# Performance work log

Measured on AMD Instinct MI355X. Metric: run time of the kernel, lower is better.

## Reference

```python
import jax, jax.numpy as jnp
import numpy as np

B, N, D, H, E = 16, 512, 256, 8, 16
DH = D // H
NEG = -1e9


def setup_inputs() -> dict:
    key = jax.random.key(0)
    ks = jax.random.split(key, 12)
    s = 0.02
    return {
        "h": jax.random.normal(ks[0], (B, N, D), dtype=jnp.float32),
        "edges": jax.random.normal(ks[1], (B, N, N, E), dtype=jnp.float32),
        "dense_mask": jnp.ones((B, N, N), dtype=bool),
        "mask": jnp.ones((B, N), dtype=bool),
        "Wq": jax.random.normal(ks[2], (D, D), dtype=jnp.float32) * s,
        "bq": jnp.zeros((D,), dtype=jnp.float32),
        "Wk": jax.random.normal(ks[3], (D, D), dtype=jnp.float32) * s,
        "bk": jnp.zeros((D,), dtype=jnp.float32),
        "Wv": jax.random.normal(ks[4], (D, D), dtype=jnp.float32) * s,
        "bv": jnp.zeros((D,), dtype=jnp.float32),
        "Wo": jax.random.normal(ks[5], (D, D), dtype=jnp.float32) * s,
        "bo": jnp.zeros((D,), dtype=jnp.float32),
        "Wp": jax.random.normal(ks[6], (E, H), dtype=jnp.float32) * s,
        "bp": jnp.zeros((H,), dtype=jnp.float32),
    }


def reference(h, edges, dense_mask, mask, Wq, bq, Wk, bk, Wv, bv, Wo, bo, Wp, bp):
    # content Q/K/V projections, split into heads
    q = (h @ Wq + bq).reshape(B, N, H, DH)
    k = (h @ Wk + bk).reshape(B, N, H, DH)
    v = (h @ Wv + bv).reshape(B, N, H, DH)
    # scaled content scores [B,H,N,N]
    scores = jnp.einsum("bnhd,bmhd->bhnm", q, k) / jnp.sqrt(jnp.float32(DH))
    # PositionAttention: per-head edge bias from the dense edge stack
    pos = jnp.einsum("bnme,eh->bhnm", edges, Wp) + bp[None, :, None, None]
    pos = pos / jnp.sqrt(jnp.float32(H))  # scale_attention
    scores = scores + pos  # merge_attention: sum (bias injected into scores)
    # fuse edge mask (dense_mask) with key padding mask (~mask is attn_mask)
    valid = dense_mask[:, None, :, :] & mask[:, None, None, :]
    scores = jnp.where(valid, scores, NEG)
    attn = jax.nn.softmax(scores, axis=-1)
    out = jnp.einsum("bhnm,bmhd->bnhd", attn, v).reshape(B, N, D)
    out = out @ Wo + bo
    return out, attn
```

## Files before the change

### kernel.cpp

```cpp
#include <hip/hip_runtime.h>
#include <hip/hip_bf16.h>

constexpr int kB = 16, kN = 512, kD = 256, kH = 8, kE = 16, kDH = 32;

typedef float f4 __attribute__((ext_vector_type(4)));
typedef __bf16 bf8 __attribute__((ext_vector_type(8)));

__device__ __forceinline__ void gload16(const void* g, const void* l) {
  __builtin_amdgcn_global_load_lds(
      (const __attribute__((address_space(1))) void*)g,
      (__attribute__((address_space(3))) void*)l, 16, 0, 0);
}

__global__ __launch_bounds__(256) void cast_h_kernel(const float* __restrict__ h,
                                                     __bf16* __restrict__ hb) {
  const int idx = (blockIdx.x * 256 + threadIdx.x) * 8;
  f4 a = *(const f4*)(h + idx);
  f4 b = *(const f4*)(h + idx + 4);
  bf8 o;
  o[0] = (__bf16)a[0]; o[1] = (__bf16)a[1]; o[2] = (__bf16)a[2]; o[3] = (__bf16)a[3];
  o[4] = (__bf16)b[0]; o[5] = (__bf16)b[1]; o[6] = (__bf16)b[2]; o[7] = (__bf16)b[3];
  *(bf8*)(hb + idx) = o;
}

__global__ __launch_bounds__(256) void prep_w_kernel(
    const float* __restrict__ Wq, const float* __restrict__ Wk,
    const float* __restrict__ Wv, const float* __restrict__ Wo,
    __bf16* __restrict__ Wt, __bf16* __restrict__ Wot) {
  const int r = blockIdx.x;
  const int t = threadIdx.x;
  if (r < 768) {
    const float* src = (r < 256) ? Wq : (r < 512) ? Wv : Wv;
    src = (r < 256) ? Wq : (r < 512) ? Wk : Wv;
    const int c = r & 255;
    Wt[(size_t)r * 256 + t] = (__bf16)src[(size_t)t * 256 + c];
  } else {
    const int rr = r - 768;
    Wot[(size_t)rr * 256 + t] = (__bf16)Wo[(size_t)t * 256 + rr];
  }
}

__global__ __launch_bounds__(256) void prep_pos_kernel(
    const float* __restrict__ edges, const int* __restrict__ dmask,
    const int* __restrict__ kmask, const float* __restrict__ Wp,
    const float* __restrict__ bp, unsigned int* __restrict__ posp) {
  const int bn = blockIdx.x;
  const int b = bn >> 9;
  const int n = bn & 511;
  const int tid = threadIdx.x;

  __shared__ __align__(16) float stg[8192];
  __shared__ __align__(16) unsigned int prow[2048];

  const float* rowg = edges + (size_t)bn * (kN * kE);

#pragma unroll
  for (int j = 0; j < 8; ++j) {
    const int L = j * 4096 + tid * 16;
    const int c = L >> 6;
    const int s = (L >> 4) & 3;
    const int e4 = s ^ (c & 3);
    gload16(rowg + c * 16 + e4 * 4, (const char*)stg + L);
  }
  __asm__ __volatile__("s_waitcnt vmcnt(0)" ::: "memory");
  __builtin_amdgcn_s_barrier();

  const float RS8 = 0.35355339059327373f;
  float bph[8];
#pragma unroll
  for (int hh = 0; hh < 8; ++hh) bph[hh] = bp[hh] * RS8;

#pragma unroll
  for (int half = 0; half < 2; ++half) {
    const int c = half * 256 + tid;
    const int dm = dmask[(size_t)bn * kN + c];
    const int km = kmask[b * kN + c];
    const bool valid = (dm != 0) && (km != 0);

    float acc[8];
#pragma unroll
    for (int hh = 0; hh < 8; ++hh) acc[hh] = 0.f;
#pragma unroll
    for (int e4 = 0; e4 < 4; ++e4) {
      const int s = e4 ^ (c & 3);
      f4 ev = *(const f4*)(stg + c * 16 + s * 4);
#pragma unroll
      for (int i = 0; i < 4; ++i) {
        const float e_ = ev[i];
#pragma unroll
        for (int hh = 0; hh < 8; ++hh)
          acc[hh] = fmaf(e_, Wp[(e4 * 4 + i) * kH + hh], acc[hh]);
      }
    }

    unsigned int w[4];
#pragma unroll
    for (int pp = 0; pp < 4; ++pp) {
      const float lo = valid ? fmaf(acc[2 * pp], RS8, bph[2 * pp]) : -1e9f;
      const float hi = valid ? fmaf(acc[2 * pp + 1], RS8, bph[2 * pp + 1]) : -1e9f;
      union { __bf16 h2[2]; unsigned int u; } pk;
      pk.h2[0] = (__bf16)lo;
      pk.h2[1] = (__bf16)hi;
      w[pp] = pk.u;
    }
    const int rot = (c + (c >> 3)) & 3;
    uint4 v;
    ((unsigned int*)&v)[0] = w[(0 - rot) & 3];
    ((unsigned int*)&v)[1] = w[(1 - rot) & 3];
    ((unsigned int*)&v)[2] = w[(2 - rot) & 3];
    ((unsigned int*)&v)[3] = w[(3 - rot) & 3];
    *(uint4*)&prow[c * 4] = v;
  }
  __builtin_amdgcn_s_barrier();

#pragma unroll
  for (int it = 0; it < 8; ++it) {
    const int li = it * 256 + tid;
    const int pp = li >> 9;
    const int m = li & 511;
    const int rot = (m + (m >> 3)) & 3;
    const unsigned int val = prow[m * 4 + ((pp + rot) & 3)];
    posp[((((size_t)(b * 4 + pp) * kN) + n) << 9) + m] = val;
  }
}

__global__ __launch_bounds__(256, 4) void qkv_gemm_kernel(
    const __bf16* __restrict__ hb, const __bf16* __restrict__ Wt,
    const float* __restrict__ bq, const float* __restrict__ bk,
    const float* __restrict__ bv,
    __bf16* __restrict__ qw, __bf16* __restrict__ kw, __bf16* __restrict__ vtw) {
  const int M0 = blockIdx.x * 128;
  const int N0 = blockIdx.y * 64;
  const int tid = threadIdx.x;
  const int wave = tid >> 6, lane = tid & 63;
  const int l15 = lane & 15, lq = lane >> 4;
  const int wm = wave & 1, wn = wave >> 1;
  const f4 fzero = {0.f, 0.f, 0.f, 0.f};

  f4 acc[4][2];
#pragma unroll
  for (int tm = 0; tm < 4; ++tm)
#pragma unroll
    for (int tn = 0; tn < 2; ++tn) acc[tm][tn] = fzero;

#pragma unroll
  for (int kk = 0; kk < 256; kk += 32) {
    bf8 af[4], bfr[2];
#pragma unroll
    for (int tm = 0; tm < 4; ++tm)
      af[tm] = *(const bf8*)(hb + (size_t)(M0 + wm * 64 + tm * 16 + l15) * 256 + kk + lq * 8);
#pragma unroll
    for (int tn = 0; tn < 2; ++tn)
      bfr[tn] = *(const bf8*)(Wt + (size_t)(N0 + wn * 32 + tn * 16 + l15) * 256 + kk + lq * 8);
#pragma unroll
    for (int tm = 0; tm < 4; ++tm)
#pragma unroll
      for (int tn = 0; tn < 2; ++tn)
        acc[tm][tn] = __builtin_amdgcn_mfma_f32_16x16x32_bf16(af[tm], bfr[tn], acc[tm][tn], 0, 0, 0);
  }

  const float QS = 0.17677669529663687f;
  const int wsel = N0 >> 8;
#pragma unroll
  for (int tn = 0; tn < 2; ++tn) {
    const int n = N0 + wn * 32 + tn * 16 + l15;
    const int c = n & 255;
    const float bias = (wsel == 0) ? bq[c] : (wsel == 1) ? bk[c] : bv[c];
#pragma unroll
    for (int tm = 0; tm < 4; ++tm) {
#pragma unroll
      for (int r = 0; r < 4; ++r) {
        const int m = M0 + wm * 64 + tm * 16 + lq * 4 + r;
        const float v = acc[tm][tn][r] + bias;
        if (wsel == 0) {
          qw[(size_t)m * 256 + c] = (__bf16)(v * QS);
        } else if (wsel == 1) {
          kw[(size_t)m * 256 + c] = (__bf16)v;
        } else {
          const int b_ = m >> 9, nn_ = m & 511, hh = c >> 5, dd = c & 31;
          vtw[(((size_t)b_ * kH + hh) * kDH + dd) * kN + nn_] = (__bf16)v;
        }
      }
    }
  }
}

__global__ __launch_bounds__(512, 2) void attn_fused_kernel(
    const __bf16* __restrict__ qw, const __bf16* __restrict__ kw,
    const __bf16* __restrict__ vtw, const unsigned int* __restrict__ posp,
    float* __restrict__ attn_out, __bf16* __restrict__ ow) {
  const int blk = blockIdx.x;
  const int b = blk >> 5;
  const int n0 = (blk & 31) * 16;
  const int tid = threadIdx.x;
  const int wave = tid >> 6, lane = tid & 63;
  const int l15 = lane & 15, lq = lane >> 4;

  __shared__ __align__(16) __bf16 p[8][16][136];

  f4 sc[32];

  const unsigned int* pw = posp + (((size_t)(b * 4 + (wave >> 1)) * kN + n0) << 9);
  const int hlo = wave & 1;
#pragma unroll
  for (int kt = 0; kt < 32; ++kt) {
#pragma unroll
    for (int r = 0; r < 4; ++r) {
      const unsigned int u = pw[(size_t)(lq * 4 + r) * kN + kt * 16 + l15];
      sc[kt][r] = __uint_as_float(hlo ? (u & 0xffff0000u) : (u << 16));
    }
  }

  bf8 qa = *(const bf8*)(qw + ((size_t)(b * kN + n0 + l15) * kH + wave) * kDH + lq * 8);
#pragma unroll
  for (int kt = 0; kt < 32; ++kt) {
    bf8 kb = *(const bf8*)(kw + ((size_t)(b * kN + kt * 16 + l15) * kH + wave) * kDH + lq * 8);
    sc[kt] = __builtin_amdgcn_mfma_f32_16x16x32_bf16(qa, kb, sc[kt], 0, 0, 0);
  }

  float inv[4];
#pragma unroll
  for (int r = 0; r < 4; ++r) {
    float m_ = sc[0][r];
#pragma unroll
    for (int kt = 1; kt < 32; ++kt) m_ = fmaxf(m_, sc[kt][r]);
#pragma unroll
    for (int s = 1; s < 16; s <<= 1) m_ = fmaxf(m_, __shfl_xor(m_, s, 16));
    float s_ = 0.f;
#pragma unroll
    for (int kt = 0; kt < 32; ++kt) {
      const float e_ = __expf(sc[kt][r] - m_);
      sc[kt][r] = e_;
      s_ += e_;
    }
#pragma unroll
    for (int s = 1; s < 16; s <<= 1) s_ += __shfl_xor(s_, s, 16);
    inv[r] = 1.0f / s_;
  }

  const f4 fzero = {0.f, 0.f, 0.f, 0.f};
  f4 oacc[2];
  oacc[0] = fzero; oacc[1] = fzero;
  float* attn_base = attn_out + ((size_t)(b * kH + wave) * kN + n0) * kN;
#pragma unroll
  for (int cc = 0; cc < 4; ++cc) {
#pragma unroll
    for (int kl = 0; kl < 8; ++kl) {
      const int kt = cc * 8 + kl;
#pragma unroll
      for (int r = 0; r < 4; ++r) {
        const float pv = sc[kt][r] * inv[r];
        attn_base[(size_t)(lq * 4 + r) * kN + kt * 16 + l15] = pv;
        p[wave][lq * 4 + r][kl * 16 + l15] = (__bf16)pv;
      }
    }
    __asm__ __volatile__("s_waitcnt lgkmcnt(0)" ::: "memory");
#pragma unroll
    for (int mc = 0; mc < 4; ++mc) {
      bf8 pa = *(const bf8*)(&p[wave][l15][mc * 32 + lq * 8]);
#pragma unroll
      for (int dd = 0; dd < 2; ++dd) {
        bf8 vb = *(const bf8*)(vtw + (((size_t)(b * kH + wave) * kDH) + dd * 16 + l15) * kN +
                               cc * 128 + mc * 32 + lq * 8);
        oacc[dd] = __builtin_amdgcn_mfma_f32_16x16x32_bf16(pa, vb, oacc[dd], 0, 0, 0);
      }
    }
  }

#pragma unroll
  for (int dd = 0; dd < 2; ++dd)
#pragma unroll
    for (int r = 0; r < 4; ++r)
      ow[(size_t)(b * kN + n0 + lq * 4 + r) * kD + wave * kDH + dd * 16 + l15] = (__bf16)oacc[dd][r];
}

__global__ __launch_bounds__(256, 4) void out_gemm_kernel(
    const __bf16* __restrict__ ob, const __bf16* __restrict__ Wot,
    const float* __restrict__ bo, float* __restrict__ out) {
  const int M0 = blockIdx.x * 128;
  const int N0 = blockIdx.y * 64;
  const int tid = threadIdx.x;
  const int wave = tid >> 6, lane = tid & 63;
  const int l15 = lane & 15, lq = lane >> 4;
  const int wm = wave & 1, wn = wave >> 1;
  const f4 fzero = {0.f, 0.f, 0.f, 0.f};

  f4 acc[4][2];
#pragma unroll
  for (int tm = 0; tm < 4; ++tm)
#pragma unroll
    for (int tn = 0; tn < 2; ++tn) acc[tm][tn] = fzero;

#pragma unroll
  for (int kk = 0; kk < 256; kk += 32) {
    bf8 af[4], bfr[2];
#pragma unroll
    for (int tm = 0; tm < 4; ++tm)
      af[tm] = *(const bf8*)(ob + (size_t)(M0 + wm * 64 + tm * 16 + l15) * 256 + kk + lq * 8);
#pragma unroll
    for (int tn = 0; tn < 2; ++tn)
      bfr[tn] = *(const bf8*)(Wot + (size_t)(N0 + wn * 32 + tn * 16 + l15) * 256 + kk + lq * 8);
#pragma unroll
    for (int tm = 0; tm < 4; ++tm)
#pragma unroll
      for (int tn = 0; tn < 2; ++tn)
        acc[tm][tn] = __builtin_amdgcn_mfma_f32_16x16x32_bf16(af[tm], bfr[tn], acc[tm][tn], 0, 0, 0);
  }

#pragma unroll
  for (int tn = 0; tn < 2; ++tn) {
    const int n = N0 + wn * 32 + tn * 16 + l15;
    const float bias = bo[n];
#pragma unroll
    for (int tm = 0; tm < 4; ++tm)
#pragma unroll
      for (int r = 0; r < 4; ++r) {
        const int m = M0 + wm * 64 + tm * 16 + lq * 4 + r;
        out[(size_t)m * 256 + n] = acc[tm][tn][r] + bias;
      }
  }
}

extern "C" void kernel_launch(void* const* d_in, const int* in_sizes, int n_in,
                              void* d_out, int out_size, void* d_ws, size_t ws_size,
                              hipStream_t stream) {
  const float* h = (const float*)d_in[0];
  const float* edges = (const float*)d_in[1];
  const int* dmask = (const int*)d_in[2];
  const int* kmask = (const int*)d_in[3];
  const float* Wq = (const float*)d_in[4];
  const float* bq = (const float*)d_in[5];
  const float* Wk = (const float*)d_in[6];
  const float* bk = (const float*)d_in[7];
  const float* Wv = (const float*)d_in[8];
  const float* bv = (const float*)d_in[9];
  const float* Wo = (const float*)d_in[10];
  const float* bo = (const float*)d_in[11];
  const float* Wp = (const float*)d_in[12];
  const float* bp = (const float*)d_in[13];

  char* ws = (char*)d_ws;
  __bf16* hb = (__bf16*)(ws);
  __bf16* Wt = (__bf16*)(ws + ((size_t)4 << 20));
  __bf16* Wot = (__bf16*)(ws + ((size_t)4 << 20) + 768 * 256 * 2);
  __bf16* qw = (__bf16*)(ws + ((size_t)5 << 20));
  __bf16* kw = (__bf16*)(ws + ((size_t)9 << 20));
  __bf16* vtw = (__bf16*)(ws + ((size_t)13 << 20));
  unsigned int* posp = (unsigned int*)(ws + ((size_t)32 << 20));
  __bf16* ow = hb;

  float* out = (float*)d_out;
  float* attn = out + (size_t)kB * kN * kD;

  cast_h_kernel<<<1024, 256, 0, stream>>>(h, hb);
  prep_w_kernel<<<1024, 256, 0, stream>>>(Wq, Wk, Wv, Wo, Wt, Wot);
  qkv_gemm_kernel<<<dim3(64, 12), 256, 0, stream>>>(hb, Wt, bq, bk, bv, qw, kw, vtw);
  prep_pos_kernel<<<kB * kN, 256, 0, stream>>>(edges, dmask, kmask, Wp, bp, posp);
  attn_fused_kernel<<<512, 512, 0, stream>>>(qw, kw, vtw, posp, attn, ow);
  out_gemm_kernel<<<dim3(64, 4), 256, 0, stream>>>(ow, Wot, bo, out);
}
```

Measured before the change: 540.1 us.

## Pre-tile position bias into MFMA fragment layout and double-buffer edge row loads

The edge-bias prep kernel now handles four query rows per block and double-buffers the edge-row loads into LDS, so the next row's global loads overlap the current row's FMA work. It writes the packed bf16 bias directly in the 16x16 MFMA accumulator fragment order as uint4s. The attention kernel can then fetch each lane's four rows with one 16-byte coalesced load instead of four scattered 4-byte loads. This removes the LDS transpose stage and the strided bias reads, at the cost of more LDS per block and fewer prep blocks.

Result: no change. 538.9 us (-0.2%).

```diff
diff --git a/kernel.cpp b/kernel.cpp
--- a/kernel.cpp
+++ b/kernel.cpp
@@ -30,8 +30,7 @@
   const int r = blockIdx.x;
   const int t = threadIdx.x;
   if (r < 768) {
-    const float* src = (r < 256) ? Wq : (r < 512) ? Wv : Wv;
-    src = (r < 256) ? Wq : (r < 512) ? Wk : Wv;
+    const float* src = (r < 256) ? Wq : (r < 512) ? Wk : Wv;
     const int c = r & 255;
     Wt[(size_t)r * 256 + t] = (__bf16)src[(size_t)t * 256 + c];
   } else {
@@ -43,84 +42,94 @@
 __global__ __launch_bounds__(256) void prep_pos_kernel(
     const float* __restrict__ edges, const int* __restrict__ dmask,
     const int* __restrict__ kmask, const float* __restrict__ Wp,
-    const float* __restrict__ bp, unsigned int* __restrict__ posp) {
-  const int bn = blockIdx.x;
-  const int b = bn >> 9;
-  const int n = bn & 511;
+    const float* __restrict__ bp, uint4* __restrict__ posp4) {
+  const int blk = blockIdx.x;
+  const int b = blk >> 7;
+  const int ng = blk & 127;
+  const int nbase = ng * 4;
   const int tid = threadIdx.x;
 
-  __shared__ __align__(16) float stg[8192];
-  __shared__ __align__(16) unsigned int prow[2048];
-
-  const float* rowg = edges + (size_t)bn * (kN * kE);
-
-#pragma unroll
-  for (int j = 0; j < 8; ++j) {
-    const int L = j * 4096 + tid * 16;
-    const int c = L >> 6;
-    const int s = (L >> 4) & 3;
-    const int e4 = s ^ (c & 3);
-    gload16(rowg + c * 16 + e4 * 4, (const char*)stg + L);
-  }
-  __asm__ __volatile__("s_waitcnt vmcnt(0)" ::: "memory");
-  __builtin_amdgcn_s_barrier();
+  __shared__ __align__(16) float stg[2][8192];
 
   const float RS8 = 0.35355339059327373f;
+
+#define ISSUE_ROW(RR, BUF)                                                        \
+  {                                                                               \
+    const float* rowg_ = edges + (size_t)(b * kN + nbase + (RR)) * (kN * kE);     \
+    _Pragma("unroll") for (int j_ = 0; j_ < 8; ++j_) {                            \
+      const int e4_ = j_ >> 1;                                                    \
+      const int c_ = (j_ & 1) * 256 + tid;                                        \
+      gload16(rowg_ + c_ * 16 + e4_ * 4,                                          \
+              (const char*)&stg[BUF][0] + j_ * 4096 + tid * 16);                  \
+    }                                                                             \
+  }
+
+  int km[2], dm[4][2];
+#pragma unroll
+  for (int half = 0; half < 2; ++half) km[half] = kmask[b * kN + half * 256 + tid];
+#pragma unroll
+  for (int rr = 0; rr < 4; ++rr)
+#pragma unroll
+    for (int half = 0; half < 2; ++half)
+      dm[rr][half] = dmask[(size_t)(b * kN + nbase + rr) * kN + half * 256 + tid];
+
   float bph[8];
 #pragma unroll
   for (int hh = 0; hh < 8; ++hh) bph[hh] = bp[hh] * RS8;
 
+  ISSUE_ROW(0, 0);
+
+  uint4 w4[2][4];
+
+#pragma unroll
+  for (int rr = 0; rr < 4; ++rr) {
+    const int buf = rr & 1;
+    __asm__ __volatile__("s_waitcnt vmcnt(0)" ::: "memory");
+    __builtin_amdgcn_s_barrier();
+    __builtin_amdgcn_sched_barrier(0);
+    if (rr < 3) ISSUE_ROW(rr + 1, buf ^ 1);
+
+#pragma unroll
+    for (int half = 0; half < 2; ++half) {
+      const int c = half * 256 + tid;
+      const bool valid = (dm[rr][half] != 0) && (km[half] != 0);
+      float acc[8];
+#pragma unroll
+      for (int hh = 0; hh < 8; ++hh) acc[hh] = 0.f;
+#pragma unroll
+      for (int e4 = 0; e4 < 4; ++e4) {
+        f4 ev = *(const f4*)(&stg[buf][e4 * 2048 + c * 4]);
+#pragma unroll
+        for (int i = 0; i < 4; ++i) {
+          const float e_ = ev[i];
+#pragma unroll
+          for (int hh = 0; hh < 8; ++hh)
+            acc[hh] = fmaf(e_, Wp[(e4 * 4 + i) * kH + hh], acc[hh]);
+        }
+      }
+#pragma unroll
+      for (int pp = 0; pp < 4; ++pp) {
+        const float lo = valid ? fmaf(acc[2 * pp], RS8, bph[2 * pp]) : -1e9f;
+        const float hi = valid ? fmaf(acc[2 * pp + 1], RS8, bph[2 * pp + 1]) : -1e9f;
+        union { __bf16 h2[2]; unsigned int u; } pk;
+        pk.h2[0] = (__bf16)lo;
+        pk.h2[1] = (__bf16)hi;
+        ((unsigned int*)&w4[half][pp])[rr] = pk.u;
+      }
+    }
+  }
+#undef ISSUE_ROW
+
+  const int nt = ng >> 2;
+  const int qq2 = ng & 3;
 #pragma unroll
   for (int half = 0; half < 2; ++half) {
     const int c = half * 256 + tid;
-    const int dm = dmask[(size_t)bn * kN + c];
-    const int km = kmask[b * kN + c];
-    const bool valid = (dm != 0) && (km != 0);
-
-    float acc[8];
-#pragma unroll
-    for (int hh = 0; hh < 8; ++hh) acc[hh] = 0.f;
-#pragma unroll
-    for (int e4 = 0; e4 < 4; ++e4) {
-      const int s = e4 ^ (c & 3);
-      f4 ev = *(const f4*)(stg + c * 16 + s * 4);
-#pragma unroll
-      for (int i = 0; i < 4; ++i) {
-        const float e_ = ev[i];
-#pragma unroll
-        for (int hh = 0; hh < 8; ++hh)
-          acc[hh] = fmaf(e_, Wp[(e4 * 4 + i) * kH + hh], acc[hh]);
-      }
-    }
-
-    unsigned int w[4];
-#pragma unroll
-    for (int pp = 0; pp < 4; ++pp) {
-      const float lo = valid ? fmaf(acc[2 * pp], RS8, bph[2 * pp]) : -1e9f;
-      const float hi = valid ? fmaf(acc[2 * pp + 1], RS8, bph[2 * pp + 1]) : -1e9f;
-      union { __bf16 h2[2]; unsigned int u; } pk;
-      pk.h2[0] = (__bf16)lo;
-      pk.h2[1] = (__bf16)hi;
-      w[pp] = pk.u;
-    }
-    const int rot = (c + (c >> 3)) & 3;
-    uint4 v;
-    ((unsigned int*)&v)[0] = w[(0 - rot) & 3];
-    ((unsigned int*)&v)[1] = w[(1 - rot) & 3];
-    ((unsigned int*)&v)[2] = w[(2 - rot) & 3];
-    ((unsigned int*)&v)[3] = w[(3 - rot) & 3];
-    *(uint4*)&prow[c * 4] = v;
-  }
-  __builtin_amdgcn_s_barrier();
-
-#pragma unroll
-  for (int it = 0; it < 8; ++it) {
-    const int li = it * 256 + tid;
-    const int pp = li >> 9;
-    const int m = li & 511;
-    const int rot = (m + (m >> 3)) & 3;
-    const unsigned int val = prow[m * 4 + ((pp + rot) & 3)];
-    posp[((((size_t)(b * 4 + pp) * kN) + n) << 9) + m] = val;
+    const size_t base =
+        ((((size_t)(b * 4) * 32 + nt) * 32 + (c >> 4)) * 64) + (c & 15) + 16 * qq2;
+#pragma unroll
+    for (int pp = 0; pp < 4; ++pp)
+      posp4[base + (size_t)pp * (32 * 32 * 64)] = w4[half][pp];
   }
 }
 
@@ -187,7 +196,7 @@
 
 __global__ __launch_bounds__(512, 2) void attn_fused_kernel(
     const __bf16* __restrict__ qw, const __bf16* __restrict__ kw,
-    const __bf16* __restrict__ vtw, const unsigned int* __restrict__ posp,
+    const __bf16* __restrict__ vtw, const uint4* __restrict__ posp4,
     float* __restrict__ attn_out, __bf16* __restrict__ ow) {
   const int blk = blockIdx.x;
   const int b = blk >> 5;
@@ -200,14 +209,21 @@
 
   f4 sc[32];
 
-  const unsigned int* pw = posp + (((size_t)(b * 4 + (wave >> 1)) * kN + n0) << 9);
+  const uint4* pw =
+      posp4 + (((size_t)(b * 4 + (wave >> 1)) * 32 + (n0 >> 4)) * 32) * 64 + lane;
   const int hlo = wave & 1;
 #pragma unroll
-  for (int kt = 0; kt < 32; ++kt) {
-#pragma unroll
-    for (int r = 0; r < 4; ++r) {
-      const unsigned int u = pw[(size_t)(lq * 4 + r) * kN + kt * 16 + l15];
-      sc[kt][r] = __uint_as_float(hlo ? (u & 0xffff0000u) : (u << 16));
+  for (int c8 = 0; c8 < 4; ++c8) {
+    uint4 u[8];
+#pragma unroll
+    for (int j = 0; j < 8; ++j) u[j] = pw[(size_t)(c8 * 8 + j) * 64];
+#pragma unroll
+    for (int j = 0; j < 8; ++j) {
+#pragma unroll
+      for (int r = 0; r < 4; ++r) {
+        const unsigned int uu = ((const unsigned int*)&u[j])[r];
+        sc[c8 * 8 + j][r] = __uint_as_float(hlo ? (uu & 0xffff0000u) : (uu << 16));
+      }
     }
   }
 
@@ -346,7 +362,7 @@
   __bf16* qw = (__bf16*)(ws + ((size_t)5 << 20));
   __bf16* kw = (__bf16*)(ws + ((size_t)9 << 20));
   __bf16* vtw = (__bf16*)(ws + ((size_t)13 << 20));
-  unsigned int* posp = (unsigned int*)(ws + ((size_t)32 << 20));
+  uint4* posp4 = (uint4*)(ws + ((size_t)32 << 20));
   __bf16* ow = hb;
 
   float* out = (float*)d_out;
@@ -355,7 +371,7 @@
   cast_h_kernel<<<1024, 256, 0, stream>>>(h, hb);
   prep_w_kernel<<<1024, 256, 0, stream>>>(Wq, Wk, Wv, Wo, Wt, Wot);
   qkv_gemm_kernel<<<dim3(64, 12), 256, 0, stream>>>(hb, Wt, bq, bk, bv, qw, kw, vtw);
-  prep_pos_kernel<<<kB * kN, 256, 0, stream>>>(edges, dmask, kmask, Wp, bp, posp);
-  attn_fused_kernel<<<512, 512, 0, stream>>>(qw, kw, vtw, posp, attn, ow);
+  prep_pos_kernel<<<kB * kN / 4, 256, 0, stream>>>(edges, dmask, kmask, Wp, bp, posp4);
+  attn_fused_kernel<<<512, 512, 0, stream>>>(qw, kw, vtw, posp4, attn, ow);
   out_gemm_kernel<<<dim3(64, 4), 256, 0, stream>>>(ow, Wot, bo, out);
 }
```
